# Kernel tuning notes

Measured on AMD Instinct MI355X. Metric: run time of the kernel, lower is better.

The kernel has to match this reference:

```python
import jax, jax.numpy as jnp
import numpy as np
from jax import lax

B, C, H, W = 256, 3, 224, 224
S = 20          # num_sample
M = 10          # mixture components
NFEAT = C + 2   # pixel channels + (x,y) loc
NHID = 100
NOUT = 10


def setup_inputs() -> dict:
    key = jax.random.key(0)
    ks = jax.random.split(key, 10)
    return {
        "x": jax.random.normal(ks[0], (B, C, H, W), jnp.float32),
        "u_cat": jax.random.uniform(ks[1], (S, B), jnp.float32),
        "z": jax.random.normal(ks[2], (S, B, 2), jnp.float32),
        "m_g_params": jax.random.normal(ks[3], (1, 6 * M), jnp.float32),
        "w_gc1": jax.random.uniform(ks[4], (NFEAT, NHID), jnp.float32, -0.1, 0.1),
        "b_gc1": jax.random.uniform(ks[5], (NHID,), jnp.float32, -0.1, 0.1),
        "w_gc2": jax.random.uniform(ks[6], (NHID, NOUT), jnp.float32, -0.3, 0.3),
        "b_gc2": jax.random.uniform(ks[7], (NOUT,), jnp.float32, -0.3, 0.3),
        "w_fcf": jax.random.uniform(ks[8], (NOUT * S, NOUT), jnp.float32, -0.07, 0.07),
        "b_fcf": jax.random.uniform(ks[9], (NOUT,), jnp.float32, -0.07, 0.07),
    }


def _forward(x, u_cat, z, m_g_params, w_gc1, b_gc1, w_gc2, b_gc2, w_fcf, b_fcf):
    # --- mixture params, replicating torch's split/stack/view reinterpretation ---
    pm = jnp.broadcast_to(m_g_params, (B, 6 * M)).reshape(B, M, 6).transpose(1, 0, 2)  # [M,B,6]
    pi = jax.nn.softmax(pm[:, :, 0].reshape(B, M), axis=-1)   # [B,M]
    mu_x = pm[:, :, 1].reshape(B, M)
    mu_y = pm[:, :, 2].reshape(B, M)
    lsig_x = pm[:, :, 3].reshape(B, M)
    lsig_y = pm[:, :, 4].reshape(B, M)
    rho = pm[:, :, 5].reshape(B, M)

    # --- categorical sampling via inverse CDF, vectorized over [S,B] ---
    cdf = jnp.cumsum(pi, axis=-1)                              # [B,M]
    idx = jnp.argmax(u_cat[:, :, None] < cdf[None, :, :], axis=-1)  # [S,B]
    bidx = jnp.arange(B)[None, :]                              # [1,B]
    mux = mu_x[bidx, idx]
    muy = mu_y[bidx, idx]
    sx = jnp.exp(lsig_x[bidx, idx])
    sy = jnp.exp(lsig_y[bidx, idx])
    r = jnp.tanh(rho[bidx, idx])

    # --- bivariate normal sample (Cholesky form); sample() is detached in torch ---
    z1, z2 = z[..., 0], z[..., 1]
    px = lax.stop_gradient(mux + sx * z1)
    py = lax.stop_gradient(muy + sy * (r * z1 + jnp.sqrt(1.0 - r * r) * z2))
    zx = (px - mux) / sx
    zy = (py - muy) / sy
    omr2 = 1.0 - r * r
    logprob = -(zx * zx - 2.0 * r * zx * zy + zy * zy) / (2.0 * omr2) \
              - jnp.log(2.0 * jnp.pi * sx * sy * jnp.sqrt(omr2))       # [S,B]
    loc = jnp.tanh(jnp.stack([px, py], axis=-1))               # [S,B,2]
    full_log_prob = jnp.sum(logprob, axis=0)                   # [B]

    # --- pixel gather (denormalize uses H for both coords, as in source) ---
    rows = jnp.clip(jnp.trunc(0.5 * (loc[..., 0] + 1.0) * H - 0.1).astype(jnp.int32), 0, H - 1)
    cols = jnp.clip(jnp.trunc(0.5 * (loc[..., 1] + 1.0) * H - 0.1).astype(jnp.int32), 0, W - 1)
    pix = x[bidx, :, rows, cols]                               # [S,B,C]

    samples = jnp.concatenate([pix, loc], axis=-1)             # [S,B,C+2]
    feat = samples.reshape(B, S, NFEAT)                        # torch .view reinterpretation

    # --- GCN with all-ones adjacency, eval mode (no dropout) ---
    adj = jnp.ones((S, S), feat.dtype)
    h = jax.nn.relu(jnp.matmul(adj, jnp.matmul(feat, w_gc1)) + b_gc1)  # [B,S,NHID]
    g = jnp.matmul(adj, jnp.matmul(h, w_gc2)) + b_gc2                  # [B,S,NOUT]
    g = jax.nn.log_softmax(g, axis=0)  # torch F.log_softmax default dim for 3D is 0

    logits = g.reshape(B, NOUT * S) @ w_fcf + b_fcf
    out = jax.nn.softmax(logits, axis=-1)                      # [B,NOUT]
    return out, full_log_prob


def reference(x, u_cat, z, m_g_params, w_gc1, b_gc1, w_gc2, b_gc2, w_fcf, b_fcf):
    return _forward(x, u_cat, z, m_g_params, w_gc1, b_gc1, w_gc2, b_gc2, w_fcf, b_fcf)
```

## Files before the change

kernel.cpp:

```cpp
#include <hip/hip_runtime.h>
#include <math.h>

#define Bn 256
#define Cn 3
#define Hn 224
#define Wn 224
#define Sn 20
#define Mn 10
#define NFEAT 5
#define NHID 100
#define NOUT 10

__global__ __launch_bounds__(256) void k_sample(
    const float* __restrict__ x, const float* __restrict__ u_cat,
    const float* __restrict__ z, const float* __restrict__ mg,
    float* __restrict__ samples, float* __restrict__ logprob)
{
    __shared__ float p[6 * Mn];
    const int b = threadIdx.x;
    const int s = blockIdx.x;
    if (b < 6 * Mn) p[b] = mg[b];
    __syncthreads();

    float raw[Mn];
#pragma unroll
    for (int m = 0; m < Mn; ++m) raw[m] = p[((b * Mn + m) >> 8) * 6 + 0];
    float mx = raw[0];
#pragma unroll
    for (int m = 1; m < Mn; ++m) mx = fmaxf(mx, raw[m]);
    float e[Mn];
    float sum = 0.f;
#pragma unroll
    for (int m = 0; m < Mn; ++m) { e[m] = expf(raw[m] - mx); sum += e[m]; }

    const float u = u_cat[s * Bn + b];
    float cdf = 0.f;
    int idx = 0;
    bool found = false;
#pragma unroll
    for (int m = 0; m < Mn; ++m) {
        cdf += e[m] / sum;
        if (!found && u < cdf) { idx = m; found = true; }
    }

    const int g = (b * Mn + idx) >> 8;
    const float mux = p[g * 6 + 1];
    const float muy = p[g * 6 + 2];
    const float sx  = expf(p[g * 6 + 3]);
    const float sy  = expf(p[g * 6 + 4]);
    const float r   = tanhf(p[g * 6 + 5]);

    const float z1 = z[(s * Bn + b) * 2 + 0];
    const float z2 = z[(s * Bn + b) * 2 + 1];

    const float px = mux + sx * z1;
    const float py = muy + sy * (r * z1 + sqrtf(1.f - r * r) * z2);
    const float zx = (px - mux) / sx;
    const float zy = (py - muy) / sy;
    const float omr2 = 1.f - r * r;
    const float lp = -(zx * zx - 2.f * r * zx * zy + zy * zy) / (2.f * omr2)
                     - logf(6.283185307179586f * sx * sy * sqrtf(omr2));

    const float lx = tanhf(px);
    const float ly = tanhf(py);

    const float vr = 0.5f * (lx + 1.f) * (float)Hn - 0.1f;
    const float vc = 0.5f * (ly + 1.f) * (float)Hn - 0.1f;
    int row = (int)vr; row = min(max(row, 0), Hn - 1);
    int col = (int)vc; col = min(max(col, 0), Wn - 1);

    const int base = (b * Cn) * (Hn * Wn) + row * Wn + col;
    const int o5 = (s * Bn + b) * NFEAT;
    samples[o5 + 0] = x[base + 0 * Hn * Wn];
    samples[o5 + 1] = x[base + 1 * Hn * Wn];
    samples[o5 + 2] = x[base + 2 * Hn * Wn];
    samples[o5 + 3] = lx;
    samples[o5 + 4] = ly;
    logprob[s * Bn + b] = lp;
}

__global__ __launch_bounds__(256) void k_head(
    const float* __restrict__ samples, const float* __restrict__ logprob,
    const float* __restrict__ w1, const float* __restrict__ b1,
    const float* __restrict__ w2, const float* __restrict__ b2,
    const float* __restrict__ wf, const float* __restrict__ bf,
    float* __restrict__ out)
{
    const int b = threadIdx.x;
    __shared__ float sh_gv[NOUT][Bn];
    __shared__ float sh_part[NOUT][16];
    __shared__ float sh_max[NOUT];
    __shared__ float sh_lse[NOUT];
    __shared__ float sh_wsum[NOUT * NOUT];

    float flp = 0.f;
#pragma unroll
    for (int s = 0; s < Sn; ++s) flp += logprob[s * Bn + b];
    out[Bn * NOUT + b] = flp;

    float fs[NFEAT] = {0.f, 0.f, 0.f, 0.f, 0.f};
    const float* sp = samples + b * Sn * NFEAT;
    for (int j = 0; j < Sn; ++j) {
#pragma unroll
        for (int f = 0; f < NFEAT; ++f) fs[f] += sp[j * NFEAT + f];
    }

    float gv[NOUT];
#pragma unroll
    for (int k = 0; k < NOUT; ++k) gv[k] = 0.f;
    for (int j = 0; j < NHID; ++j) {
        float a = b1[j];
#pragma unroll
        for (int f = 0; f < NFEAT; ++f) a += fs[f] * w1[f * NHID + j];
        const float h = fmaxf(a, 0.f);
#pragma unroll
        for (int k = 0; k < NOUT; ++k) gv[k] += h * w2[j * NOUT + k];
    }
#pragma unroll
    for (int k = 0; k < NOUT; ++k) {
        gv[k] = (float)Sn * gv[k] + b2[k];
        sh_gv[k][b] = gv[k];
    }

    if (b < NOUT * NOUT) {
        const int k = b / NOUT, o = b % NOUT;
        float w = 0.f;
        for (int s = 0; s < Sn; ++s) w += wf[(s * NOUT + k) * NOUT + o];
        sh_wsum[b] = w;
    }
    __syncthreads();

    if (b < NOUT * 16) {
        const int k = b >> 4, part = b & 15;
        float m0 = sh_gv[k][part * 16];
        for (int i = 1; i < 16; ++i) m0 = fmaxf(m0, sh_gv[k][part * 16 + i]);
        sh_part[k][part] = m0;
    }
    __syncthreads();
    if (b < NOUT) {
        float m0 = sh_part[b][0];
        for (int i = 1; i < 16; ++i) m0 = fmaxf(m0, sh_part[b][i]);
        sh_max[b] = m0;
    }
    __syncthreads();
    if (b < NOUT * 16) {
        const int k = b >> 4, part = b & 15;
        const float m0 = sh_max[k];
        float sacc = 0.f;
        for (int i = 0; i < 16; ++i) sacc += expf(sh_gv[k][part * 16 + i] - m0);
        sh_part[k][part] = sacc;
    }
    __syncthreads();
    if (b < NOUT) {
        float sacc = 0.f;
        for (int i = 0; i < 16; ++i) sacc += sh_part[b][i];
        sh_lse[b] = sh_max[b] + logf(sacc);
    }
    __syncthreads();

    float lg[NOUT];
#pragma unroll
    for (int k = 0; k < NOUT; ++k) lg[k] = gv[k] - sh_lse[k];
    float logits[NOUT];
#pragma unroll
    for (int o = 0; o < NOUT; ++o) {
        float a = bf[o];
#pragma unroll
        for (int k = 0; k < NOUT; ++k) a += lg[k] * sh_wsum[k * NOUT + o];
        logits[o] = a;
    }
    float mxl = logits[0];
#pragma unroll
    for (int o = 1; o < NOUT; ++o) mxl = fmaxf(mxl, logits[o]);
    float ssum = 0.f;
#pragma unroll
    for (int o = 0; o < NOUT; ++o) { logits[o] = expf(logits[o] - mxl); ssum += logits[o]; }
#pragma unroll
    for (int o = 0; o < NOUT; ++o) out[b * NOUT + o] = logits[o] / ssum;
}

extern "C" void kernel_launch(void* const* d_in, const int* in_sizes, int n_in,
                              void* d_out, int out_size, void* d_ws, size_t ws_size,
                              hipStream_t stream) {
    const float* x   = (const float*)d_in[0];
    const float* u   = (const float*)d_in[1];
    const float* z   = (const float*)d_in[2];
    const float* mg  = (const float*)d_in[3];
    const float* w1  = (const float*)d_in[4];
    const float* b1  = (const float*)d_in[5];
    const float* w2  = (const float*)d_in[6];
    const float* b2  = (const float*)d_in[7];
    const float* wf  = (const float*)d_in[8];
    const float* bf  = (const float*)d_in[9];
    float* out = (float*)d_out;

    float* samples = (float*)d_ws;
    float* logprob = samples + Sn * Bn * NFEAT;

    hipLaunchKernelGGL(k_sample, dim3(Sn), dim3(Bn), 0, stream,
                       x, u, z, mg, samples, logprob);
    hipLaunchKernelGGL(k_head, dim3(1), dim3(Bn), 0, stream,
                       samples, logprob, w1, b1, w2, b2, wf, bf, out);
}
```

Baseline: 237.5 us.

## Fuse sampling and GCN head into a single one-block kernel

Merges the sampling kernel and the head kernel into one launch of a single 256-thread block. Each thread handles the 20 samples that map to its row after the view reinterpretation and accumulates pixel and location features directly, so the samples buffer is no longer written to and read back from global memory. Log-probs go to shared memory, and per-component constants are precomputed once. This removes a kernel launch and the global round trip, but it serialises the 5120 scattered gathers from x onto one block, losing the 20-block parallelism of the old sampling stage.

Measured after the change: 291.3 us. 22.6% more time.

```diff
diff --git a/kernel.cpp b/kernel.cpp
--- a/kernel.cpp
+++ b/kernel.cpp
@@ -11,122 +11,128 @@
 #define NHID 100
 #define NOUT 10
 
-__global__ __launch_bounds__(256) void k_sample(
+__global__ __launch_bounds__(256) void k_fused(
     const float* __restrict__ x, const float* __restrict__ u_cat,
     const float* __restrict__ z, const float* __restrict__ mg,
-    float* __restrict__ samples, float* __restrict__ logprob)
-{
-    __shared__ float p[6 * Mn];
-    const int b = threadIdx.x;
-    const int s = blockIdx.x;
-    if (b < 6 * Mn) p[b] = mg[b];
-    __syncthreads();
-
-    float raw[Mn];
-#pragma unroll
-    for (int m = 0; m < Mn; ++m) raw[m] = p[((b * Mn + m) >> 8) * 6 + 0];
-    float mx = raw[0];
-#pragma unroll
-    for (int m = 1; m < Mn; ++m) mx = fmaxf(mx, raw[m]);
-    float e[Mn];
-    float sum = 0.f;
-#pragma unroll
-    for (int m = 0; m < Mn; ++m) { e[m] = expf(raw[m] - mx); sum += e[m]; }
-
-    const float u = u_cat[s * Bn + b];
-    float cdf = 0.f;
-    int idx = 0;
-    bool found = false;
-#pragma unroll
-    for (int m = 0; m < Mn; ++m) {
-        cdf += e[m] / sum;
-        if (!found && u < cdf) { idx = m; found = true; }
-    }
-
-    const int g = (b * Mn + idx) >> 8;
-    const float mux = p[g * 6 + 1];
-    const float muy = p[g * 6 + 2];
-    const float sx  = expf(p[g * 6 + 3]);
-    const float sy  = expf(p[g * 6 + 4]);
-    const float r   = tanhf(p[g * 6 + 5]);
-
-    const float z1 = z[(s * Bn + b) * 2 + 0];
-    const float z2 = z[(s * Bn + b) * 2 + 1];
-
-    const float px = mux + sx * z1;
-    const float py = muy + sy * (r * z1 + sqrtf(1.f - r * r) * z2);
-    const float zx = (px - mux) / sx;
-    const float zy = (py - muy) / sy;
-    const float omr2 = 1.f - r * r;
-    const float lp = -(zx * zx - 2.f * r * zx * zy + zy * zy) / (2.f * omr2)
-                     - logf(6.283185307179586f * sx * sy * sqrtf(omr2));
-
-    const float lx = tanhf(px);
-    const float ly = tanhf(py);
-
-    const float vr = 0.5f * (lx + 1.f) * (float)Hn - 0.1f;
-    const float vc = 0.5f * (ly + 1.f) * (float)Hn - 0.1f;
-    int row = (int)vr; row = min(max(row, 0), Hn - 1);
-    int col = (int)vc; col = min(max(col, 0), Wn - 1);
-
-    const int base = (b * Cn) * (Hn * Wn) + row * Wn + col;
-    const int o5 = (s * Bn + b) * NFEAT;
-    samples[o5 + 0] = x[base + 0 * Hn * Wn];
-    samples[o5 + 1] = x[base + 1 * Hn * Wn];
-    samples[o5 + 2] = x[base + 2 * Hn * Wn];
-    samples[o5 + 3] = lx;
-    samples[o5 + 4] = ly;
-    logprob[s * Bn + b] = lp;
-}
-
-__global__ __launch_bounds__(256) void k_head(
-    const float* __restrict__ samples, const float* __restrict__ logprob,
     const float* __restrict__ w1, const float* __restrict__ b1,
     const float* __restrict__ w2, const float* __restrict__ b2,
     const float* __restrict__ wf, const float* __restrict__ bf,
     float* __restrict__ out)
 {
     const int b = threadIdx.x;
+
+    __shared__ float p[6 * Mn];
+    __shared__ float cdf[Bn][Mn];
+    __shared__ float bk[Mn][8];
+    __shared__ float lp_arr[Sn * Bn];
     __shared__ float sh_gv[NOUT][Bn];
     __shared__ float sh_part[NOUT][16];
     __shared__ float sh_max[NOUT];
     __shared__ float sh_lse[NOUT];
     __shared__ float sh_wsum[NOUT * NOUT];
 
-    float flp = 0.f;
-#pragma unroll
-    for (int s = 0; s < Sn; ++s) flp += logprob[s * Bn + b];
-    out[Bn * NOUT + b] = flp;
-
-    float fs[NFEAT] = {0.f, 0.f, 0.f, 0.f, 0.f};
-    const float* sp = samples + b * Sn * NFEAT;
-    for (int j = 0; j < Sn; ++j) {
-#pragma unroll
-        for (int f = 0; f < NFEAT; ++f) fs[f] += sp[j * NFEAT + f];
-    }
-
-    float gv[NOUT];
-#pragma unroll
-    for (int k = 0; k < NOUT; ++k) gv[k] = 0.f;
-    for (int j = 0; j < NHID; ++j) {
-        float a = b1[j];
-#pragma unroll
-        for (int f = 0; f < NFEAT; ++f) a += fs[f] * w1[f * NHID + j];
-        const float h = fmaxf(a, 0.f);
-#pragma unroll
-        for (int k = 0; k < NOUT; ++k) gv[k] += h * w2[j * NOUT + k];
-    }
-#pragma unroll
-    for (int k = 0; k < NOUT; ++k) {
-        gv[k] = (float)Sn * gv[k] + b2[k];
-        sh_gv[k][b] = gv[k];
-    }
-
+    if (b < 6 * Mn) p[b] = mg[b];
+    __syncthreads();
+
+    {
+        float raw[Mn];
+#pragma unroll
+        for (int m = 0; m < Mn; ++m) raw[m] = p[((b * Mn + m) >> 8) * 6 + 0];
+        float mx = raw[0];
+#pragma unroll
+        for (int m = 1; m < Mn; ++m) mx = fmaxf(mx, raw[m]);
+        float e[Mn];
+        float sum = 0.f;
+#pragma unroll
+        for (int m = 0; m < Mn; ++m) { e[m] = expf(raw[m] - mx); sum += e[m]; }
+        float c = 0.f;
+#pragma unroll
+        for (int m = 0; m < Mn; ++m) { c += e[m] / sum; cdf[b][m] = c; }
+    }
+    if (b < Mn) {
+        const float mux = p[b * 6 + 1];
+        const float muy = p[b * 6 + 2];
+        const float sx  = expf(p[b * 6 + 3]);
+        const float sy  = expf(p[b * 6 + 4]);
+        const float r   = tanhf(p[b * 6 + 5]);
+        const float omr2 = 1.f - r * r;
+        const float sq = sqrtf(omr2);
+        bk[b][0] = mux; bk[b][1] = muy; bk[b][2] = sx; bk[b][3] = sy;
+        bk[b][4] = r;   bk[b][5] = sq;
+        bk[b][6] = logf(6.283185307179586f * sx * sy * sq);
+    }
     if (b < NOUT * NOUT) {
         const int k = b / NOUT, o = b % NOUT;
         float w = 0.f;
         for (int s = 0; s < Sn; ++s) w += wf[(s * NOUT + k) * NOUT + o];
         sh_wsum[b] = w;
+    }
+    __syncthreads();
+
+    float fs[NFEAT] = {0.f, 0.f, 0.f, 0.f, 0.f};
+    for (int sp = 0; sp < Sn; ++sp) {
+        const int t  = b * Sn + sp;
+        const int bo = t & (Bn - 1);
+
+        const float u = u_cat[t];
+        int idx = 0;
+        bool found = false;
+#pragma unroll
+        for (int m = 0; m < Mn; ++m) {
+            if (!found && u < cdf[bo][m]) { idx = m; found = true; }
+        }
+        const int g = (bo * Mn + idx) >> 8;
+
+        const float mux = bk[g][0], muy = bk[g][1];
+        const float sx = bk[g][2], sy = bk[g][3];
+        const float r = bk[g][4], sq = bk[g][5], lterm = bk[g][6];
+
+        const float z1 = z[t * 2 + 0];
+        const float z2 = z[t * 2 + 1];
+
+        const float px = mux + sx * z1;
+        const float py = muy + sy * (r * z1 + sq * z2);
+        const float zx = (px - mux) / sx;
+        const float zy = (py - muy) / sy;
+        const float omr2 = 1.f - r * r;
+        lp_arr[t] = -(zx * zx - 2.f * r * zx * zy + zy * zy) / (2.f * omr2) - lterm;
+
+        const float lx = tanhf(px);
+        const float ly = tanhf(py);
+        const float vr = 0.5f * (lx + 1.f) * (float)Hn - 0.1f;
+        const float vc = 0.5f * (ly + 1.f) * (float)Hn - 0.1f;
+        int row = (int)vr; row = min(max(row, 0), Hn - 1);
+        int col = (int)vc; col = min(max(col, 0), Wn - 1);
+
+        const int base = bo * Cn * Hn * Wn + row * Wn + col;
+        fs[0] += x[base + 0 * Hn * Wn];
+        fs[1] += x[base + 1 * Hn * Wn];
+        fs[2] += x[base + 2 * Hn * Wn];
+        fs[3] += lx;
+        fs[4] += ly;
+    }
+    __syncthreads();
+
+    float flp = 0.f;
+#pragma unroll
+    for (int s = 0; s < Sn; ++s) flp += lp_arr[s * Bn + b];
+    out[Bn * NOUT + b] = flp;
+
+    float gv[NOUT];
+#pragma unroll
+    for (int k = 0; k < NOUT; ++k) gv[k] = 0.f;
+    for (int j = 0; j < NHID; ++j) {
+        float a = b1[j];
+#pragma unroll
+        for (int f = 0; f < NFEAT; ++f) a += fs[f] * w1[f * NHID + j];
+        const float h = fmaxf(a, 0.f);
+#pragma unroll
+        for (int k = 0; k < NOUT; ++k) gv[k] += h * w2[j * NOUT + k];
+    }
+#pragma unroll
+    for (int k = 0; k < NOUT; ++k) {
+        gv[k] = (float)Sn * gv[k] + b2[k];
+        sh_gv[k][b] = gv[k];
     }
     __syncthreads();
 
@@ -194,11 +200,6 @@
     const float* bf  = (const float*)d_in[9];
     float* out = (float*)d_out;
 
-    float* samples = (float*)d_ws;
-    float* logprob = samples + Sn * Bn * NFEAT;
-
-    hipLaunchKernelGGL(k_sample, dim3(Sn), dim3(Bn), 0, stream,
-                       x, u, z, mg, samples, logprob);
-    hipLaunchKernelGGL(k_head, dim3(1), dim3(Bn), 0, stream,
-                       samples, logprob, w1, b1, w2, b2, wf, bf, out);
+    hipLaunchKernelGGL(k_fused, dim3(1), dim3(Bn), 0, stream,
+                       x, u, z, mg, w1, b1, w2, b2, wf, bf, out);
 }
```

## Spread sampling over more small blocks, precompute mixture params, vectorize head loads

Applied to the files above, without the earlier changes.

The sampling kernel now launches 80 blocks of 64 threads instead of 20 blocks of 256, so the dependent pixel gathers are spread across more compute units. The per-component exp/tanh/sqrt/log terms are computed once per block into shared memory rather than per thread. The head kernel reads each batch row's 100 sample floats as 25 float4 loads instead of scalar loads. The extra barrier and shared-memory setup are repeated in every small block, and the float4 reads assume the workspace rows are 16-byte aligned, which holds since each row is 100 floats.

Result: no change. 235.0 us (-1.1%).

```diff
diff --git a/kernel.cpp b/kernel.cpp
--- a/kernel.cpp
+++ b/kernel.cpp
@@ -10,21 +10,37 @@
 #define NFEAT 5
 #define NHID 100
 #define NOUT 10
-
-__global__ __launch_bounds__(256) void k_sample(
+#define NT (Sn * Bn)
+
+__global__ __launch_bounds__(64) void k_sample(
     const float* __restrict__ x, const float* __restrict__ u_cat,
     const float* __restrict__ z, const float* __restrict__ mg,
     float* __restrict__ samples, float* __restrict__ logprob)
 {
     __shared__ float p[6 * Mn];
-    const int b = threadIdx.x;
-    const int s = blockIdx.x;
-    if (b < 6 * Mn) p[b] = mg[b];
+    __shared__ float bk[Mn][8];
+    const int lt = threadIdx.x;
+    const int t  = blockIdx.x * 64 + lt;
+    const int bo = t & (Bn - 1);
+
+    if (lt < 6 * Mn) p[lt] = mg[lt];
+    __syncthreads();
+    if (lt < Mn) {
+        const float mux = p[lt * 6 + 1];
+        const float muy = p[lt * 6 + 2];
+        const float sx  = expf(p[lt * 6 + 3]);
+        const float sy  = expf(p[lt * 6 + 4]);
+        const float r   = tanhf(p[lt * 6 + 5]);
+        const float sq  = sqrtf(1.f - r * r);
+        bk[lt][0] = mux; bk[lt][1] = muy; bk[lt][2] = sx; bk[lt][3] = sy;
+        bk[lt][4] = r;   bk[lt][5] = sq;
+        bk[lt][6] = logf(6.283185307179586f * sx * sy * sq);
+    }
     __syncthreads();
 
     float raw[Mn];
 #pragma unroll
-    for (int m = 0; m < Mn; ++m) raw[m] = p[((b * Mn + m) >> 8) * 6 + 0];
+    for (int m = 0; m < Mn; ++m) raw[m] = p[((bo * Mn + m) >> 8) * 6 + 0];
     float mx = raw[0];
 #pragma unroll
     for (int m = 1; m < Mn; ++m) mx = fmaxf(mx, raw[m]);
@@ -33,50 +49,45 @@
 #pragma unroll
     for (int m = 0; m < Mn; ++m) { e[m] = expf(raw[m] - mx); sum += e[m]; }
 
-    const float u = u_cat[s * Bn + b];
-    float cdf = 0.f;
+    const float u = u_cat[t];
+    float c = 0.f;
     int idx = 0;
     bool found = false;
 #pragma unroll
     for (int m = 0; m < Mn; ++m) {
-        cdf += e[m] / sum;
-        if (!found && u < cdf) { idx = m; found = true; }
-    }
-
-    const int g = (b * Mn + idx) >> 8;
-    const float mux = p[g * 6 + 1];
-    const float muy = p[g * 6 + 2];
-    const float sx  = expf(p[g * 6 + 3]);
-    const float sy  = expf(p[g * 6 + 4]);
-    const float r   = tanhf(p[g * 6 + 5]);
-
-    const float z1 = z[(s * Bn + b) * 2 + 0];
-    const float z2 = z[(s * Bn + b) * 2 + 1];
+        c += e[m] / sum;
+        if (!found && u < c) { idx = m; found = true; }
+    }
+    const int g = (bo * Mn + idx) >> 8;
+
+    const float mux = bk[g][0], muy = bk[g][1];
+    const float sx = bk[g][2], sy = bk[g][3];
+    const float r = bk[g][4], sq = bk[g][5], lterm = bk[g][6];
+
+    const float z1 = z[t * 2 + 0];
+    const float z2 = z[t * 2 + 1];
 
     const float px = mux + sx * z1;
-    const float py = muy + sy * (r * z1 + sqrtf(1.f - r * r) * z2);
+    const float py = muy + sy * (r * z1 + sq * z2);
     const float zx = (px - mux) / sx;
     const float zy = (py - muy) / sy;
     const float omr2 = 1.f - r * r;
-    const float lp = -(zx * zx - 2.f * r * zx * zy + zy * zy) / (2.f * omr2)
-                     - logf(6.283185307179586f * sx * sy * sqrtf(omr2));
+    logprob[t] = -(zx * zx - 2.f * r * zx * zy + zy * zy) / (2.f * omr2) - lterm;
 
     const float lx = tanhf(px);
     const float ly = tanhf(py);
-
     const float vr = 0.5f * (lx + 1.f) * (float)Hn - 0.1f;
     const float vc = 0.5f * (ly + 1.f) * (float)Hn - 0.1f;
     int row = (int)vr; row = min(max(row, 0), Hn - 1);
     int col = (int)vc; col = min(max(col, 0), Wn - 1);
 
-    const int base = (b * Cn) * (Hn * Wn) + row * Wn + col;
-    const int o5 = (s * Bn + b) * NFEAT;
+    const int base = bo * Cn * Hn * Wn + row * Wn + col;
+    const int o5 = t * NFEAT;
     samples[o5 + 0] = x[base + 0 * Hn * Wn];
     samples[o5 + 1] = x[base + 1 * Hn * Wn];
     samples[o5 + 2] = x[base + 2 * Hn * Wn];
     samples[o5 + 3] = lx;
     samples[o5 + 4] = ly;
-    logprob[s * Bn + b] = lp;
 }
 
 __global__ __launch_bounds__(256) void k_head(
@@ -99,10 +110,14 @@
     out[Bn * NOUT + b] = flp;
 
     float fs[NFEAT] = {0.f, 0.f, 0.f, 0.f, 0.f};
-    const float* sp = samples + b * Sn * NFEAT;
-    for (int j = 0; j < Sn; ++j) {
-#pragma unroll
-        for (int f = 0; f < NFEAT; ++f) fs[f] += sp[j * NFEAT + f];
+    const float4* sp4 = (const float4*)(samples + b * Sn * NFEAT);
+#pragma unroll
+    for (int v = 0; v < 25; ++v) {
+        const float4 q = sp4[v];
+        fs[(v * 4 + 0) % NFEAT] += q.x;
+        fs[(v * 4 + 1) % NFEAT] += q.y;
+        fs[(v * 4 + 2) % NFEAT] += q.z;
+        fs[(v * 4 + 3) % NFEAT] += q.w;
     }
 
     float gv[NOUT];
@@ -195,9 +210,9 @@
     float* out = (float*)d_out;
 
     float* samples = (float*)d_ws;
-    float* logprob = samples + Sn * Bn * NFEAT;
-
-    hipLaunchKernelGGL(k_sample, dim3(Sn), dim3(Bn), 0, stream,
+    float* logprob = samples + NT * NFEAT;
+
+    hipLaunchKernelGGL(k_sample, dim3(NT / 64), dim3(64), 0, stream,
                        x, u, z, mg, samples, logprob);
     hipLaunchKernelGGL(k_head, dim3(1), dim3(Bn), 0, stream,
                        samples, logprob, w1, b1, w2, b2, wf, bf, out);
```
